# Kernel optimization log

Hardware: AMD Instinct MI355X
Metric: run time of the kernel (lower is better)

Reference implementation:

```python
import jax, jax.numpy as jnp
import numpy as np

B, S, D_IN = 2, 2048, 2048
H, G, HD = 16, 4, 128          # heads, kv groups, head_dim
GS = H // G                    # group size (heads per kv group)
EPS = 1e-6
SCALE = HD ** -0.5


def rms_norm(x, w):
    # RMSNorm over last dim (head_dim)
    var = jnp.mean(jnp.square(x), axis=-1, keepdims=True)
    return x * jax.lax.rsqrt(var + EPS) * w


def apply_rope(x, cos, sin):
    # x: [b, h, s, d]; cos/sin: [s, d]. Rotate-half convention.
    d = x.shape[-1]
    x1, x2 = x[..., : d // 2], x[..., d // 2 :]
    rotated = jnp.concatenate([-x2, x1], axis=-1)
    return x * cos[None, None] + rotated * sin[None, None]


def setup_inputs() -> dict:
    key = jax.random.key(0)
    ks = jax.random.split(key, 8)
    x = jax.random.normal(ks[0], (B, S, D_IN), jnp.float32)
    mask = jnp.triu(jnp.ones((S, S), jnp.bool_), k=1)  # True = masked (future)
    # realistic RoPE tables
    inv_freq = 1.0 / (10000.0 ** (jnp.arange(0, HD, 2, dtype=jnp.float32) / HD))
    angles = jnp.arange(S, dtype=jnp.float32)[:, None] * inv_freq[None, :]  # [S, HD/2]
    angles = jnp.concatenate([angles, angles], axis=-1)  # [S, HD]
    cos, sin = jnp.cos(angles), jnp.sin(angles)
    sd = 0.02
    Wq = jax.random.normal(ks[1], (D_IN, H * HD), jnp.float32) * sd
    Wk = jax.random.normal(ks[2], (D_IN, G * HD), jnp.float32) * sd
    Wv = jax.random.normal(ks[3], (D_IN, G * HD), jnp.float32) * sd
    Wo = jax.random.normal(ks[4], (H * HD, D_IN), jnp.float32) * sd
    q_norm_w = jnp.ones((HD,), jnp.float32)
    k_norm_w = jnp.ones((HD,), jnp.float32)
    return {"x": x, "mask": mask, "cos": cos, "sin": sin, "Wq": Wq, "Wk": Wk,
            "Wv": Wv, "Wo": Wo, "q_norm_w": q_norm_w, "k_norm_w": k_norm_w}


def reference(x, mask, cos, sin, Wq, Wk, Wv, Wo, q_norm_w, k_norm_w):
    b, s, _ = x.shape
    q = (x @ Wq).reshape(b, s, H, HD).transpose(0, 2, 1, 3)   # [b,H,s,d]
    k = (x @ Wk).reshape(b, s, G, HD).transpose(0, 2, 1, 3)   # [b,G,s,d]
    v = (x @ Wv).reshape(b, s, G, HD).transpose(0, 2, 1, 3)   # [b,G,s,d]
    q = rms_norm(q, q_norm_w)
    k = rms_norm(k, k_norm_w)
    q = apply_rope(q, cos, sin)
    k = apply_rope(k, cos, sin)
    q = q * SCALE
    # GQA without materializing repeated KV: split heads into [G, GS]
    qg = q.reshape(b, G, GS, s, HD)                           # [b,G,gs,s,d]
    scores = jnp.einsum('bghsd,bgtd->bghst', qg, k)           # [b,G,gs,s,s]
    scores = jnp.where(mask[None, None, None], -jnp.inf, scores)
    attn = jax.nn.softmax(scores, axis=-1)
    ctx = jnp.einsum('bghst,bgtd->bghsd', attn, v)            # [b,G,gs,s,d]
    ctx = ctx.reshape(b, H, s, HD).transpose(0, 2, 1, 3).reshape(b, s, H * HD)
    return ctx @ Wo
```

## Files before the change

### kernel.cpp

```cpp
#include <hip/hip_runtime.h>
#include <cstdint>
#include <cstddef>

typedef unsigned short u16;
typedef __bf16 bf16x8 __attribute__((ext_vector_type(8)));
typedef float f32x4 __attribute__((ext_vector_type(4)));

#define SLEN 2048
#define NHEADS 16
#define NGRP 4

__device__ inline float bf2f(u16 u) { return __uint_as_float(((unsigned)u) << 16); }
__device__ inline u16 f2bf(float f) {
    unsigned u = __float_as_uint(f);
    u += 0x7fffu + ((u >> 16) & 1u);
    return (u16)(u >> 16);
}

__device__ inline f32x4 mfma16(bf16x8 a, bf16x8 b, f32x4 c) {
    return __builtin_amdgcn_mfma_f32_16x16x32_bf16(a, b, c, 0, 0, 0);
}

__device__ inline void memfence_compiler() { __asm__ volatile("" ::: "memory"); }

__device__ inline void cp16(const u16* g, u16* l) {
    __builtin_amdgcn_global_load_lds(
        (__attribute__((address_space(1))) void*)(u16*)g,
        (__attribute__((address_space(3))) void*)l, 16, 0, 0);
}


__device__ inline void transpose_f32_body(u16 (*tile)[65], const float* __restrict__ in,
                                          u16* __restrict__ out, int R, int C, int bx, int by,
                                          int tid) {
    const long r0 = (long)by * 64, c0 = (long)bx * 64;
    for (int j = 0; j < 4; j++) {
        int c = j * 256 + tid;
        int lr = c >> 4, lc = (c & 15) * 4;
        float4 v = *(const float4*)&in[(r0 + lr) * (long)C + c0 + lc];
        tile[lr][lc + 0] = f2bf(v.x); tile[lr][lc + 1] = f2bf(v.y);
        tile[lr][lc + 2] = f2bf(v.z); tile[lr][lc + 3] = f2bf(v.w);
    }
    __syncthreads();
    for (int j = 0; j < 4; j++) {
        int c = j * 256 + tid;
        int orow = c >> 4, oc = (c & 15) * 4;
        ushort4 vv;
        vv.x = tile[oc + 0][orow]; vv.y = tile[oc + 1][orow];
        vv.z = tile[oc + 2][orow]; vv.w = tile[oc + 3][orow];
        *(ushort4*)&out[(c0 + orow) * (long)R + r0 + oc] = vv;
    }
}

__device__ inline void transpose_bf_body(u16 (*tile)[65], const u16* __restrict__ in, long inRS,
                                         u16* __restrict__ out, int R, int C, int bx, int by,
                                         int tid) {
    const long r0 = (long)by * 64, c0 = (long)bx * 64;
    for (int j = 0; j < 4; j++) {
        int c = j * 256 + tid;
        int lr = c >> 4, lc = (c & 15) * 4;
        ushort4 vv = *(const ushort4*)&in[(r0 + lr) * inRS + c0 + lc];
        tile[lr][lc + 0] = vv.x; tile[lr][lc + 1] = vv.y;
        tile[lr][lc + 2] = vv.z; tile[lr][lc + 3] = vv.w;
    }
    __syncthreads();
    for (int j = 0; j < 4; j++) {
        int c = j * 256 + tid;
        int orow = c >> 4, oc = (c & 15) * 4;
        ushort4 vv;
        vv.x = tile[oc + 0][orow]; vv.y = tile[oc + 1][orow];
        vv.z = tile[oc + 2][orow]; vv.w = tile[oc + 3][orow];
        *(ushort4*)&out[(c0 + orow) * (long)R + r0 + oc] = vv;
    }
}

__device__ inline void normrope_body(u16* __restrict__ buf, long rowstride, int heads,
                                     const u16* __restrict__ w,
                                     const float* __restrict__ cosf, const float* __restrict__ sinf,
                                     float scale, int row, int lane) {
    u16* p = buf + (long)(row / heads) * rowstride + (row % heads) * 128;
    float x1 = bf2f(p[lane]);
    float x2 = bf2f(p[lane + 64]);
    float ss = x1 * x1 + x2 * x2;
    for (int off = 1; off < 64; off <<= 1) ss += __shfl_xor(ss, off);
    float inv = rsqrtf(ss * (1.f / 128.f) + 1e-6f);
    int s = (row / heads) % SLEN;
    float c1 = cosf[s * 128 + lane], c2 = cosf[s * 128 + 64 + lane];
    float s1 = sinf[s * 128 + lane], s2 = sinf[s * 128 + 64 + lane];
    float w1 = bf2f(w[lane]), w2 = bf2f(w[lane + 64]);
    float y1 = x1 * inv * w1, y2 = x2 * inv * w2;
    p[lane]      = f2bf((y1 * c1 - y2 * s1) * scale);
    p[lane + 64] = f2bf((y2 * c2 + y1 * s2) * scale);
}

__global__ __launch_bounds__(256) void prep_k(const float* __restrict__ x, u16* __restrict__ xbf,
                                              const float* __restrict__ qw, const float* __restrict__ kw,
                                              u16* qwb, u16* kwb,
                                              const float* __restrict__ Wq, const float* __restrict__ Wk,
                                              const float* __restrict__ Wv, u16* __restrict__ wqkvT) {
    __shared__ u16 tile[64][65];
    const int bid = blockIdx.x, tid = threadIdx.x;
    if (bid < 8192) {
        long i = ((long)bid * 256 + tid) * 4;
        float4 v = *(const float4*)(x + i);
        ushort4 o;
        o.x = f2bf(v.x); o.y = f2bf(v.y); o.z = f2bf(v.z); o.w = f2bf(v.w);
        *(ushort4*)(xbf + i) = o;
    } else if (bid == 8192) {
        if (tid < 128) qwb[tid] = f2bf(qw[tid]);
        else kwb[tid - 128] = f2bf(kw[tid - 128]);
    } else if (bid < 9217) {
        int rem = bid - 8193;
        transpose_f32_body(tile, Wq, wqkvT, 2048, 2048, rem & 31, rem >> 5, tid);
    } else if (bid < 9473) {
        int rem = bid - 9217;
        transpose_f32_body(tile, Wk, wqkvT + 2048L * 2048, 2048, 512, rem & 7, rem >> 3, tid);
    } else {
        int rem = bid - 9473;
        transpose_f32_body(tile, Wv, wqkvT + 2560L * 2048, 2048, 512, rem & 7, rem >> 3, tid);
    }
}

__global__ __launch_bounds__(256) void mid_k(u16* __restrict__ qkvb, u16* __restrict__ vTb,
                                             const u16* __restrict__ qwb, const u16* __restrict__ kwb,
                                             const float* __restrict__ cosf, const float* __restrict__ sinf,
                                             const float* __restrict__ Wo, u16* __restrict__ woT) {
    __shared__ u16 tile[64][65];
    const int bid = blockIdx.x, tid = threadIdx.x;
    if (bid < 512) {
        transpose_bf_body(tile, qkvb + 2560, 3072L, vTb, 4096, 512, bid & 7, bid >> 3, tid);
    } else if (bid < 16896) {
        int row = (bid - 512) * 4 + (tid >> 6);
        normrope_body(qkvb, 3072L, NHEADS, qwb, cosf, sinf, 0.08838834764831845f, row, tid & 63);
    } else if (bid < 20992) {
        int row = (bid - 16896) * 4 + (tid >> 6);
        normrope_body(qkvb + 2048, 3072L, NGRP, kwb, cosf, sinf, 1.0f, row, tid & 63);
    } else {
        int rem = bid - 20992;
        transpose_f32_body(tile, Wo, woT, 2048, 2048, rem & 31, rem >> 5, tid);
    }
}

template <typename OutT, int NI>
__global__ __launch_bounds__(512, 2) void gemm8p(const u16* __restrict__ A, const u16* __restrict__ Bt,
                                                 OutT* __restrict__ C, int N, int K) {
    extern __shared__ u16 smem[];
    constexpr int AUNIT = 8192;
    constexpr int BUNIT = NI * 2048;
    constexpr int GATE = 2 + NI / 2;
    const int tid = threadIdx.x;
    const int lane = tid & 63, wave = tid >> 6;
    const int l15 = lane & 15, quad = lane >> 4;
    const int wm = (wave >> 2) * 128, wn = (wave & 3) * (NI * 16);
    const long m0 = (long)blockIdx.y * 256, n0 = (long)blockIdx.x * (NI * 64);

    f32x4 acc[8][NI];
    #pragma unroll
    for (int i = 0; i < 8; i++)
        #pragma unroll
        for (int j = 0; j < NI; j++) acc[i][j] = {0.f, 0.f, 0.f, 0.f};

    const u16* aBase = A + m0 * (long)K;
    const u16* bBase = Bt + n0 * (long)K;

    auto stageA = [&](int kt, int c, int k) {
        u16* dst = smem + (c * 2 + k) * AUNIT + wave * 512;
        #pragma unroll
        for (int i = 0; i < 2; i++) {
            int cd = i * 512 + wave * 64 + lane;
            int r = cd >> 2;
            int js = (cd & 3) ^ ((r >> 1) & 3);
            cp16(aBase + (long)r * K + kt + k * 32 + js * 8, dst + i * 4096);
        }
    };
    auto stageB = [&](int kt, int c, int k) {
        u16* dst = smem + 4 * AUNIT + (c * 2 + k) * BUNIT + wave * 512;
        #pragma unroll
        for (int i = 0; i < NI / 2; i++) {
            int cd = i * 512 + wave * 64 + lane;
            int r = cd >> 2;
            int js = (cd & 3) ^ ((r >> 1) & 3);
            cp16(bBase + (long)r * K + kt + k * 32 + js * 8, dst + i * 4096);
        }
    };

    stageA(0, 0, 0); stageB(0, 0, 0); stageA(0, 0, 1); stageB(0, 0, 1);

    const int nkt = K >> 6;

    for (int t = 0; t < nkt; ++t) {
        const int c = t & 1;
        const int kt1 = (t + 1) << 6;
        const bool more = (t + 1) < nkt;
        #pragma unroll
        for (int k = 0; k < 2; ++k) {
            if (k == 0 || more) {
                if constexpr (NI == 4) asm volatile("s_waitcnt vmcnt(4)" ::: "memory");
                else                   asm volatile("s_waitcnt vmcnt(3)" ::: "memory");
            } else {
                asm volatile("s_waitcnt vmcnt(0)" ::: "memory");
            }
            __builtin_amdgcn_s_barrier();

            const u16* au = smem + (c * 2 + k) * AUNIT;
            const u16* bu = smem + 4 * AUNIT + (c * 2 + k) * BUNIT;

            bf16x8 bfr[NI], af[4];
            #pragma unroll
            for (int ni = 0; ni < NI; ni++) {
                const int r = wn + ni * 16 + l15;
                bfr[ni] = *(const bf16x8*)&bu[r * 32 + (quad ^ ((r >> 1) & 3)) * 8];
            }
            #pragma unroll
            for (int mi = 0; mi < 4; mi++) {
                const int r = wm + mi * 16 + l15;
                af[mi] = *(const bf16x8*)&au[r * 32 + (quad ^ ((r >> 1) & 3)) * 8];
            }
            if (more) stageA(kt1, c ^ 1, k);
            asm volatile("s_waitcnt lgkmcnt(0)" ::: "memory");
            __builtin_amdgcn_sched_barrier(0);
            __builtin_amdgcn_s_setprio(1);
            #pragma unroll
            for (int mi = 0; mi < 4; mi++)
                #pragma unroll
                for (int ni = 0; ni < NI; ni++)
                    acc[mi][ni] = mfma16(af[mi], bfr[ni], acc[mi][ni]);
            __builtin_amdgcn_s_setprio(0);
            __builtin_amdgcn_s_barrier();

            #pragma unroll
            for (int mi = 0; mi < 4; mi++) {
                const int r = wm + 64 + mi * 16 + l15;
                af[mi] = *(const bf16x8*)&au[r * 32 + (quad ^ ((r >> 1) & 3)) * 8];
            }
            if (more) stageB(kt1, c ^ 1, k);
            asm volatile("s_waitcnt lgkmcnt(0)" ::: "memory");
            __builtin_amdgcn_sched_barrier(0);
            __builtin_amdgcn_s_setprio(1);
            #pragma unroll
            for (int mi = 0; mi < 4; mi++)
                #pragma unroll
                for (int ni = 0; ni < NI; ni++)
                    acc[4 + mi][ni] = mfma16(af[mi], bfr[ni], acc[4 + mi][ni]);
            __builtin_amdgcn_s_setprio(0);
            __builtin_amdgcn_s_barrier();
        }
    }

    #pragma unroll
    for (int mi = 0; mi < 8; mi++)
        #pragma unroll
        for (int r = 0; r < 4; r++) {
            long row = m0 + wm + mi * 16 + quad * 4 + r;
            OutT* crow = C + row * (long)N + n0 + wn + l15;
            #pragma unroll
            for (int ni = 0; ni < NI; ni++) {
                float v = acc[mi][ni][r];
                if constexpr (sizeof(OutT) == 2) crow[ni * 16] = f2bf(v);
                else crow[ni * 16] = v;
            }
        }
}

__global__ __launch_bounds__(256, 2) void attn(const u16* __restrict__ qkv, const u16* __restrict__ vT,
                                               u16* __restrict__ ctx) {
    __shared__ u16 KB[64 * 128];
    __shared__ u16 VB[128 * 64];
    __shared__ u16 Ps[4][2][16][72];
    __shared__ float Al[4][2][16];
    const int tid = threadIdx.x;
    const int lane = tid & 63, wave = tid >> 6;
    const int l15 = lane & 15, quad = lane >> 4;
    const int bg = blockIdx.x & 7, b = bg >> 2, g = bg & 3;
    const int rest = blockIdx.x >> 3;
    const int h = g * 4 + (rest & 3);
    const int idx = rest >> 2;
    const int qt = (idx < 8) ? (15 - idx) : (idx - 8);
    const int wr = qt * 128 + wave * 32;

    union { bf16x8 v; u16 s[8]; } uo;
    for (int j = 0; j < 8; j++) uo.s[j] = 0x3F80;
    const bf16x8 ones = uo.v;

    bf16x8 qa[2][4];
    for (int m = 0; m < 2; m++) {
        const u16* qp = qkv + (long)(b * SLEN + wr + m * 16 + l15) * 3072 + h * 128 + quad * 8;
        for (int kc = 0; kc < 4; kc++) qa[m][kc] = *(const bf16x8*)(qp + kc * 32);
    }
    float m_i[2] = {-__builtin_inff(), -__builtin_inff()};
    f32x4 l_acc[2];
    f32x4 o[2][8];
    for (int m = 0; m < 2; m++) l_acc[m] = {0.f, 0.f, 0.f, 0.f};
    for (int m = 0; m < 2; m++)
        for (int nf = 0; nf < 8; nf++) o[m][nf] = {0.f, 0.f, 0.f, 0.f};

    const u16* kqb = qkv + (long)b * SLEN * 3072 + 2048 + g * 128;
    const u16* vgb = vT + (long)g * 128 * 4096 + (long)b * SLEN;
    const int xk = (l15 & 7) << 4;
    const int nt = 2 * qt + 2;

    for (int t = 0; t < nt; ++t) {
        const int t0 = t * 64;
        #pragma unroll
        for (int i = 0; i < 4; ++i) {
            const int j = wave * 4 + i;
            {
                const int row = j * 4 + (lane >> 4);
                const int cs = lane & 15;
                cp16(kqb + (long)(t0 + row) * 3072 + ((cs ^ (row & 7)) * 8), &KB[j * 512]);
            }
            {
                const int row = j * 8 + (lane >> 3);
                const int cs = lane & 7;
                cp16(vgb + (long)row * 4096 + t0 + ((cs ^ (row & 7)) * 8), &VB[j * 512]);
            }
        }
        __syncthreads();

        if (t0 <= wr + 31) {
            bf16x8 kf[4][4];
            #pragma unroll
            for (int nf = 0; nf < 4; nf++)
                #pragma unroll
                for (int kc = 0; kc < 4; kc++)
                    kf[nf][kc] = *(const bf16x8*)((const char*)KB +
                                  (nf * 16 + l15) * 256 + ((quad * 16 + kc * 64) ^ xk));

            f32x4 sc[2][4];
            for (int m = 0; m < 2; m++)
                for (int nf = 0; nf < 4; nf++) sc[m][nf] = {0.f, 0.f, 0.f, 0.f};
            #pragma unroll
            for (int kc = 0; kc < 4; kc++)
                #pragma unroll
                for (int nf = 0; nf < 4; nf++) {
                    sc[0][nf] = mfma16(kf[nf][kc], qa[0][kc], sc[0][nf]);
                    sc[1][nf] = mfma16(kf[nf][kc], qa[1][kc], sc[1][nf]);
                }
            if (t0 + 63 > wr) {
                #pragma unroll
                for (int m = 0; m < 2; m++) {
                    int qrow = wr + m * 16 + l15;
                    #pragma unroll
                    for (int nf = 0; nf < 4; nf++)
                        #pragma unroll
                        for (int r = 0; r < 4; r++)
                            if (t0 + nf * 16 + quad * 4 + r > qrow) sc[m][nf][r] = -__builtin_inff();
                }
            }
            float alpha[2];
            #pragma unroll
            for (int m = 0; m < 2; m++) {
                float mx = sc[m][0][0];
                #pragma unroll
                for (int nf = 0; nf < 4; nf++)
                    #pragma unroll
                    for (int r = 0; r < 4; r++) mx = fmaxf(mx, sc[m][nf][r]);
                mx = fmaxf(mx, __shfl_xor(mx, 16));
                mx = fmaxf(mx, __shfl_xor(mx, 32));
                float mn = fmaxf(m_i[m], mx);
                alpha[m] = __expf(m_i[m] - mn);
                m_i[m] = mn;
                Al[wave][m][l15] = alpha[m];
            }
            #pragma unroll
            for (int m = 0; m < 2; m++)
                #pragma unroll
                for (int nf = 0; nf < 4; nf++) {
                    ushort4 pk;
                    pk.x = f2bf(__expf(sc[m][nf][0] - m_i[m]));
                    pk.y = f2bf(__expf(sc[m][nf][1] - m_i[m]));
                    pk.z = f2bf(__expf(sc[m][nf][2] - m_i[m]));
                    pk.w = f2bf(__expf(sc[m][nf][3] - m_i[m]));
                    *(ushort4*)&Ps[wave][m][l15][nf * 16 + quad * 4] = pk;
                }
            memfence_compiler();
            f32x4 al[2];
            al[0] = *(const f32x4*)&Al[wave][0][quad * 4];
            al[1] = *(const f32x4*)&Al[wave][1][quad * 4];
            #pragma unroll
            for (int m = 0; m < 2; m++) {
                #pragma unroll
                for (int nf = 0; nf < 8; nf++)
                    #pragma unroll
                    for (int r = 0; r < 4; r++) o[m][nf][r] *= al[m][r];
                #pragma unroll
                for (int r = 0; r < 4; r++) l_acc[m][r] *= al[m][r];
            }
            {
                bf16x8 vf[8];
                #pragma unroll
                for (int nf = 0; nf < 8; nf++)
                    vf[nf] = *(const bf16x8*)((const char*)VB +
                              (nf * 16 + l15) * 128 + ((quad * 16) ^ xk));
                bf16x8 pa0 = *(const bf16x8*)&Ps[wave][0][l15][quad * 8];
                bf16x8 pa1 = *(const bf16x8*)&Ps[wave][1][l15][quad * 8];
                #pragma unroll
                for (int nf = 0; nf < 8; nf++) {
                    o[0][nf] = mfma16(pa0, vf[nf], o[0][nf]);
                    o[1][nf] = mfma16(pa1, vf[nf], o[1][nf]);
                }
                l_acc[0] = mfma16(pa0, ones, l_acc[0]);
                l_acc[1] = mfma16(pa1, ones, l_acc[1]);
            }
            {
                bf16x8 vf[8];
                #pragma unroll
                for (int nf = 0; nf < 8; nf++)
                    vf[nf] = *(const bf16x8*)((const char*)VB +
                              (nf * 16 + l15) * 128 + ((64 + quad * 16) ^ xk));
                bf16x8 pa0 = *(const bf16x8*)&Ps[wave][0][l15][32 + quad * 8];
                bf16x8 pa1 = *(const bf16x8*)&Ps[wave][1][l15][32 + quad * 8];
                #pragma unroll
                for (int nf = 0; nf < 8; nf++) {
                    o[0][nf] = mfma16(pa0, vf[nf], o[0][nf]);
                    o[1][nf] = mfma16(pa1, vf[nf], o[1][nf]);
                }
                l_acc[0] = mfma16(pa0, ones, l_acc[0]);
                l_acc[1] = mfma16(pa1, ones, l_acc[1]);
            }
            memfence_compiler();
        }
        __syncthreads();
    }

    #pragma unroll
    for (int m = 0; m < 2; m++)
        #pragma unroll
        for (int r = 0; r < 4; r++) {
            float inv = 1.f / l_acc[m][r];
            int srow = wr + m * 16 + quad * 4 + r;
            u16* cp = ctx + (long)(b * SLEN + srow) * 2048 + h * 128 + l15;
            #pragma unroll
            for (int nf = 0; nf < 8; nf++) cp[nf * 16] = f2bf(o[m][nf][r] * inv);
        }
}

extern "C" void kernel_launch(void* const* d_in, const int* in_sizes, int n_in,
                              void* d_out, int out_size, void* d_ws, size_t ws_size,
                              hipStream_t stream) {
    const float* x    = (const float*)d_in[0];
    const float* cosi = (const float*)d_in[2];
    const float* sini = (const float*)d_in[3];
    const float* Wq   = (const float*)d_in[4];
    const float* Wk   = (const float*)d_in[5];
    const float* Wv   = (const float*)d_in[6];
    const float* Wo   = (const float*)d_in[7];
    const float* qw   = (const float*)d_in[8];
    const float* kw   = (const float*)d_in[9];
    float* out = (float*)d_out;
    char* ws = (char*)d_ws;

    const size_t MB = 1 << 20;
    u16* qkvb  = (u16*)(ws);
    u16* vTb   = (u16*)(ws + 24 * MB);
    u16* xbf   = (u16*)(ws + 28 * MB);
    u16* ctx   = (u16*)(ws + 28 * MB);
    u16* wqkvT = (u16*)(ws + 44 * MB);
    u16* woT   = (u16*)(ws + 44 * MB);
    u16* qwb   = (u16*)(ws + 56 * MB);
    u16* kwb   = (u16*)(ws + 56 * MB + 256);

    prep_k<<<9729, 256, 0, stream>>>(x, xbf, qw, kw, qwb, kwb, Wq, Wk, Wv, wqkvT);

    gemm8p<u16, 4><<<dim3(12, 16), 512, 131072, stream>>>(xbf, wqkvT, qkvb, 3072, 2048);

    mid_k<<<22016, 256, 0, stream>>>(qkvb, vTb, qwb, kwb, cosi, sini, Wo, woT);

    attn<<<dim3(512, 1, 1), 256, 0, stream>>>(qkvb, vTb, ctx);

    gemm8p<float, 2><<<dim3(16, 16), 512, 98304, stream>>>(ctx, woT, out, 2048, 2048);
}
```

Before: 320.2 us.

## Remap GEMM blocks across XCDs, prefetch both A halves, load V directly into registers

The GEMM now remaps the linear workgroup id so consecutive tiles land on the same XCD chunk, aiming to improve L2 reuse. It also loads both halves of the A fragments up front and waits only partially on LDS, so the second half's loads overlap the first MFMA batch. In attention, V is no longer staged through shared memory. Each wave loads its V fragments straight from global memory into registers, which removes LDS traffic but adds register pressure and uncoalesced global reads duplicated across waves.

```diff
diff --git a/kernel.cpp b/kernel.cpp
--- a/kernel.cpp
+++ b/kernel.cpp
@@ -147,12 +147,16 @@
     extern __shared__ u16 smem[];
     constexpr int AUNIT = 8192;
     constexpr int BUNIT = NI * 2048;
-    constexpr int GATE = 2 + NI / 2;
     const int tid = threadIdx.x;
     const int lane = tid & 63, wave = tid >> 6;
     const int l15 = lane & 15, quad = lane >> 4;
     const int wm = (wave >> 2) * 128, wn = (wave & 3) * (NI * 16);
-    const long m0 = (long)blockIdx.y * 256, n0 = (long)blockIdx.x * (NI * 64);
+
+    const int nbx = gridDim.x;
+    const int nwg = nbx * gridDim.y;
+    const int d = blockIdx.y * nbx + blockIdx.x;
+    const int s = (d & 7) * (nwg >> 3) + (d >> 3);
+    const long m0 = (long)(s / nbx) * 256, n0 = (long)(s % nbx) * (NI * 64);
 
     f32x4 acc[8][NI];
     #pragma unroll
@@ -205,7 +209,7 @@
             const u16* au = smem + (c * 2 + k) * AUNIT;
             const u16* bu = smem + 4 * AUNIT + (c * 2 + k) * BUNIT;
 
-            bf16x8 bfr[NI], af[4];
+            bf16x8 bfr[NI], af0[4], af1[4];
             #pragma unroll
             for (int ni = 0; ni < NI; ni++) {
                 const int r = wn + ni * 16 + l15;
@@ -214,25 +218,25 @@
             #pragma unroll
             for (int mi = 0; mi < 4; mi++) {
                 const int r = wm + mi * 16 + l15;
-                af[mi] = *(const bf16x8*)&au[r * 32 + (quad ^ ((r >> 1) & 3)) * 8];
+                af0[mi] = *(const bf16x8*)&au[r * 32 + (quad ^ ((r >> 1) & 3)) * 8];
+            }
+            #pragma unroll
+            for (int mi = 0; mi < 4; mi++) {
+                const int r = wm + 64 + mi * 16 + l15;
+                af1[mi] = *(const bf16x8*)&au[r * 32 + (quad ^ ((r >> 1) & 3)) * 8];
             }
             if (more) stageA(kt1, c ^ 1, k);
-            asm volatile("s_waitcnt lgkmcnt(0)" ::: "memory");
+            asm volatile("s_waitcnt lgkmcnt(4)" ::: "memory");
             __builtin_amdgcn_sched_barrier(0);
             __builtin_amdgcn_s_setprio(1);
             #pragma unroll
             for (int mi = 0; mi < 4; mi++)
                 #pragma unroll
                 for (int ni = 0; ni < NI; ni++)
-                    acc[mi][ni] = mfma16(af[mi], bfr[ni], acc[mi][ni]);
+                    acc[mi][ni] = mfma16(af0[mi], bfr[ni], acc[mi][ni]);
             __builtin_amdgcn_s_setprio(0);
             __builtin_amdgcn_s_barrier();
 
-            #pragma unroll
-            for (int mi = 0; mi < 4; mi++) {
-                const int r = wm + 64 + mi * 16 + l15;
-                af[mi] = *(const bf16x8*)&au[r * 32 + (quad ^ ((r >> 1) & 3)) * 8];
-            }
             if (more) stageB(kt1, c ^ 1, k);
             asm volatile("s_waitcnt lgkmcnt(0)" ::: "memory");
             __builtin_amdgcn_sched_barrier(0);
@@ -241,7 +245,7 @@
             for (int mi = 0; mi < 4; mi++)
                 #pragma unroll
                 for (int ni = 0; ni < NI; ni++)
-                    acc[4 + mi][ni] = mfma16(af[mi], bfr[ni], acc[4 + mi][ni]);
+                    acc[4 + mi][ni] = mfma16(af1[mi], bfr[ni], acc[4 + mi][ni]);
             __builtin_amdgcn_s_setprio(0);
             __builtin_amdgcn_s_barrier();
         }
@@ -265,7 +269,6 @@
 __global__ __launch_bounds__(256, 2) void attn(const u16* __restrict__ qkv, const u16* __restrict__ vT,
                                                u16* __restrict__ ctx) {
     __shared__ u16 KB[64 * 128];
-    __shared__ u16 VB[128 * 64];
     __shared__ u16 Ps[4][2][16][72];
     __shared__ float Al[4][2][16];
     const int tid = threadIdx.x;
@@ -301,23 +304,26 @@
 
     for (int t = 0; t < nt; ++t) {
         const int t0 = t * 64;
+        const bool live = (t0 <= wr + 31);
         #pragma unroll
         for (int i = 0; i < 4; ++i) {
             const int j = wave * 4 + i;
-            {
-                const int row = j * 4 + (lane >> 4);
-                const int cs = lane & 15;
-                cp16(kqb + (long)(t0 + row) * 3072 + ((cs ^ (row & 7)) * 8), &KB[j * 512]);
-            }
-            {
-                const int row = j * 8 + (lane >> 3);
-                const int cs = lane & 7;
-                cp16(vgb + (long)row * 4096 + t0 + ((cs ^ (row & 7)) * 8), &VB[j * 512]);
-            }
+            const int row = j * 4 + (lane >> 4);
+            const int cs = lane & 15;
+            cp16(kqb + (long)(t0 + row) * 3072 + ((cs ^ (row & 7)) * 8), &KB[j * 512]);
+        }
+        bf16x8 vf0[8], vf1[8];
+        if (live) {
+            #pragma unroll
+            for (int nf = 0; nf < 8; nf++)
+                vf0[nf] = *(const bf16x8*)(vgb + (long)(nf * 16 + l15) * 4096 + t0 + quad * 8);
+            #pragma unroll
+            for (int nf = 0; nf < 8; nf++)
+                vf1[nf] = *(const bf16x8*)(vgb + (long)(nf * 16 + l15) * 4096 + t0 + 32 + quad * 8);
         }
         __syncthreads();
 
-        if (t0 <= wr + 31) {
+        if (live) {
             bf16x8 kf[4][4];
             #pragma unroll
             for (int nf = 0; nf < 4; nf++)
@@ -387,33 +393,23 @@
                 for (int r = 0; r < 4; r++) l_acc[m][r] *= al[m][r];
             }
             {
-                bf16x8 vf[8];
-                #pragma unroll
-                for (int nf = 0; nf < 8; nf++)
-                    vf[nf] = *(const bf16x8*)((const char*)VB +
-                              (nf * 16 + l15) * 128 + ((quad * 16) ^ xk));
                 bf16x8 pa0 = *(const bf16x8*)&Ps[wave][0][l15][quad * 8];
                 bf16x8 pa1 = *(const bf16x8*)&Ps[wave][1][l15][quad * 8];
                 #pragma unroll
                 for (int nf = 0; nf < 8; nf++) {
-                    o[0][nf] = mfma16(pa0, vf[nf], o[0][nf]);
-                    o[1][nf] = mfma16(pa1, vf[nf], o[1][nf]);
+                    o[0][nf] = mfma16(pa0, vf0[nf], o[0][nf]);
+                    o[1][nf] = mfma16(pa1, vf0[nf], o[1][nf]);
                 }
                 l_acc[0] = mfma16(pa0, ones, l_acc[0]);
                 l_acc[1] = mfma16(pa1, ones, l_acc[1]);
             }
             {
-                bf16x8 vf[8];
-                #pragma unroll
-                for (int nf = 0; nf < 8; nf++)
-                    vf[nf] = *(const bf16x8*)((const char*)VB +
-                              (nf * 16 + l15) * 128 + ((64 + quad * 16) ^ xk));
                 bf16x8 pa0 = *(const bf16x8*)&Ps[wave][0][l15][32 + quad * 8];
                 bf16x8 pa1 = *(const bf16x8*)&Ps[wave][1][l15][32 + quad * 8];
                 #pragma unroll
                 for (int nf = 0; nf < 8; nf++) {
-                    o[0][nf] = mfma16(pa0, vf[nf], o[0][nf]);
-                    o[1][nf] = mfma16(pa1, vf[nf], o[1][nf]);
+                    o[0][nf] = mfma16(pa0, vf1[nf], o[0][nf]);
+                    o[1][nf] = mfma16(pa1, vf1[nf], o[1][nf]);
                 }
                 l_acc[0] = mfma16(pa0, ones, l_acc[0]);
                 l_acc[1] = mfma16(pa1, ones, l_acc[1]);
```

Measured after the change: 378.1 us. +18.1%, slower.
